# Optimization experiments

Measured on AMD Instinct MI355X. Metric: run time of the kernel, lower is better.

The kernel has to match this reference:

```python
import jax, jax.numpy as jnp
import numpy as np

EPS = 1e-7


def squash(s):
    # safe norm over last axis, keepdims
    norm = jnp.sqrt(jnp.sum(jnp.square(s), axis=-1, keepdims=True) + EPS)
    norm_sq = jnp.square(norm)
    return norm_sq / (1.0 + norm_sq) / norm * s


def setup_inputs() -> dict:
    key = jax.random.key(0)
    k1, k2 = jax.random.split(key)
    B, IN_CAPS, IN_DIM = 64, 2048, 16
    N_CAPS, CAP_DIM = 64, 16
    x = jax.random.normal(k1, (B, IN_CAPS, IN_DIM), dtype=jnp.float32)
    # glorot-uniform-ish init for W
    limit = (6.0 / (IN_DIM + N_CAPS * CAP_DIM)) ** 0.5
    W = jax.random.uniform(k2, (IN_CAPS, IN_DIM, N_CAPS * CAP_DIM),
                           minval=-limit, maxval=limit, dtype=jnp.float32)
    bias = jnp.zeros((N_CAPS, CAP_DIM), dtype=jnp.float32)
    return {"x": x, "W": W, "bias": bias}


def reference(x, W, bias):
    B, in_caps, in_dim = x.shape
    n_caps, cap_dim = bias.shape
    r_iters = 3
    # projection: [B, in_caps, n_caps*cap_dim] -> [B, in_caps, n_caps, cap_dim]
    u_hat = jnp.einsum('bij,ijk->bik', x, W).reshape(B, in_caps, n_caps, cap_dim)
    b = jnp.zeros((B, in_caps, n_caps, 1), dtype=u_hat.dtype)
    v = None
    for r in range(r_iters):
        c = jax.nn.softmax(b, axis=2)                       # route over class caps
        s = jnp.sum(u_hat * c, axis=1, keepdims=True)       # [B, 1, n_caps, cap_dim]
        s = s + bias
        v = squash(s)
        if r < r_iters - 1:
            agreement = jnp.sum(u_hat * v, axis=-1, keepdims=True)
            b = b + agreement
    return jnp.squeeze(v, axis=1)                           # [B, n_caps, cap_dim]
```

## Files before the change

### kernel.cpp

```cpp
#include <hip/hip_runtime.h>
#include <hip/hip_fp16.h>
#include <cstdio>

#define B_  64
#define I_  2048
#define J_  16
#define N_  64
#define D_  16
#define K_  1024

typedef __attribute__((ext_vector_type(2))) float float2v;

#if __has_builtin(__builtin_amdgcn_cvt_pk_u8_f32)
#define CVTPK_U8(f, sel, old) (unsigned)__builtin_amdgcn_cvt_pk_u8_f32((f), (sel), (old))
#else
__device__ __forceinline__ unsigned cvtpk_u8_sw(float f, unsigned sel, unsigned old) {
  unsigned b = (unsigned)(int)f & 0xffu;
  unsigned sh = sel * 8u;
  return (old & ~(0xffu << sh)) | (b << sh);
}
#define CVTPK_U8(f, sel, old) cvtpk_u8_sw((f), (sel), (old))
#endif

__device__ __forceinline__ void pk_fma_lo(float2v& a, float2v x, float2v w) {
  asm("v_pk_fma_f32 %0, %1, %2, %0 op_sel:[0,0,0] op_sel_hi:[0,1,1]"
      : "+v"(a) : "v"(x), "v"(w));
}
__device__ __forceinline__ void pk_fma_hi(float2v& a, float2v x, float2v w) {
  asm("v_pk_fma_f32 %0, %1, %2, %0 op_sel:[1,0,0] op_sel_hi:[1,1,1]"
      : "+v"(a) : "v"(x), "v"(w));
}

__global__ __launch_bounds__(256, 3) void project_k(const float* __restrict__ x,
                                                    const float* __restrict__ W,
                                                    unsigned char* __restrict__ uh,
                                                    unsigned short* __restrict__ sc) {
  const int i  = blockIdx.x >> 1;
  const int b0 = (blockIdx.x & 1) * 32;
  const int t  = threadIdx.x;

  __shared__ float4 xl4[32 * 4];
  if (t < 128) {
    int bb = t >> 2, q = t & 3;
    xl4[t] = ((const float4*)(x + ((size_t)(b0 + bb) * I_ + i) * J_))[q];
  }

  const float4* Wp = (const float4*)(W + (size_t)i * (J_ * K_));
  float2v w2[32];
#pragma unroll
  for (int j = 0; j < J_; ++j) {
    float4 wv = Wp[j * (K_ / 4) + t];
    w2[2 * j]     = float2v{wv.x, wv.y};
    w2[2 * j + 1] = float2v{wv.z, wv.w};
  }
  __syncthreads();

  unsigned char*  op  = uh + ((size_t)b0 * I_ + i) * K_ + t * 4;
  unsigned short* scp = sc + ((size_t)b0 * I_ + i) * N_ + (t >> 2);
  const bool lead = (t & 3) == 0;
  const float2v* xlp = (const float2v*)xl4;

#define QUANT_STORE(A01, A23) do {                                              \
    float ax_ = fmaxf(fmaxf(fabsf((A01).x), fabsf((A01).y)),                    \
                      fmaxf(fabsf((A23).x), fabsf((A23).y)));                   \
    ax_ = fmaxf(ax_, __shfl_xor(ax_, 1));                                       \
    ax_ = fmaxf(ax_, __shfl_xor(ax_, 2));                                       \
    float inv_ = __fdividef(127.0f, fmaxf(ax_, 1e-30f));                        \
    float e0_ = rintf(fmaf((A01).x, inv_, 128.f));                              \
    float e1_ = rintf(fmaf((A01).y, inv_, 128.f));                              \
    float e2_ = rintf(fmaf((A23).x, inv_, 128.f));                              \
    float e3_ = rintf(fmaf((A23).y, inv_, 128.f));                              \
    unsigned pk_ = CVTPK_U8(e0_, 0u, 0u);                                       \
    pk_ = CVTPK_U8(e1_, 1u, pk_);                                               \
    pk_ = CVTPK_U8(e2_, 2u, pk_);                                               \
    pk_ = CVTPK_U8(e3_, 3u, pk_);                                               \
    *(unsigned int*)op = pk_;                                                   \
    if (lead) *scp = __half_as_ushort(__float2half_rn(ax_ * (1.0f / 127.0f))); \
    op  += (size_t)I_ * K_;                                                     \
    scp += (size_t)I_ * N_;                                                     \
  } while (0)

#define FMA_BODY(XP)                                                            \
    float2v a01 = {0.f, 0.f}, a23 = {0.f, 0.f};                                 \
    _Pragma("unroll")                                                           \
    for (int p = 0; p < 8; ++p) {                                               \
      pk_fma_lo(a01, (XP)[p], w2[4 * p + 0]);                                   \
      pk_fma_lo(a23, (XP)[p], w2[4 * p + 1]);                                   \
      pk_fma_hi(a01, (XP)[p], w2[4 * p + 2]);                                   \
      pk_fma_hi(a23, (XP)[p], w2[4 * p + 3]);                                   \
    }

  float2v xa[8], xb[8];
#pragma unroll
  for (int p = 0; p < 8; ++p) xa[p] = xlp[p];

  for (int bb = 0; bb < 32; bb += 2) {
#pragma unroll
    for (int p = 0; p < 8; ++p) xb[p] = xlp[(bb + 1) * 8 + p];
    {
      FMA_BODY(xa)
      QUANT_STORE(a01, a23);
    }
    if (bb + 2 < 32) {
#pragma unroll
      for (int p = 0; p < 8; ++p) xa[p] = xlp[(bb + 2) * 8 + p];
    }
    {
      FMA_BODY(xb)
      QUANT_STORE(a01, a23);
    }
  }
#undef FMA_BODY
#undef QUANT_STORE
}

template <int MODE>
__global__ __launch_bounds__(256, 4) void route_k(const unsigned char* __restrict__ uh,
                                                  const unsigned short* __restrict__ sc,
                                                  const float* __restrict__ sa,
                                                  const float* __restrict__ sb,
                                                  const float* __restrict__ bias,
                                                  float* __restrict__ s_out) {
  const int t    = threadIdx.x;
  const int lane = t & 63;
  const int wv   = t >> 6;
  const int b    = blockIdx.x >> 4;
  const int iw   = ((blockIdx.x & 15) << 2) + wv;
  const int i0   = iw * 32;

  float vsum[16];
  float voff = 0.f;
  if (MODE >= 1) {
    float bs[16];
#pragma unroll
    for (int q = 0; q < 4; ++q) {
      float4 bb4 = *(const float4*)&bias[lane * 16 + q * 4];
      bs[q*4+0] = bb4.x; bs[q*4+1] = bb4.y; bs[q*4+2] = bb4.z; bs[q*4+3] = bb4.w;
    }
    {
      float va[16], nn = 0.f;
#pragma unroll
      for (int q = 0; q < 4; ++q) {
        float4 tmp = *(const float4*)&sa[(size_t)b * K_ + lane * 16 + q * 4];
        va[q*4+0] = tmp.x + bs[q*4+0]; va[q*4+1] = tmp.y + bs[q*4+1];
        va[q*4+2] = tmp.z + bs[q*4+2]; va[q*4+3] = tmp.w + bs[q*4+3];
      }
#pragma unroll
      for (int d = 0; d < 16; ++d) nn += va[d] * va[d];
      float n2 = nn + 1e-7f;
      float f = sqrtf(n2) / (1.0f + n2);
#pragma unroll
      for (int d = 0; d < 16; ++d) vsum[d] = va[d] * f;
    }
    if (MODE == 2) {
      float vb[16], nn = 0.f;
#pragma unroll
      for (int q = 0; q < 4; ++q) {
        float4 tmp = *(const float4*)&sb[(size_t)b * K_ + lane * 16 + q * 4];
        vb[q*4+0] = tmp.x + bs[q*4+0]; vb[q*4+1] = tmp.y + bs[q*4+1];
        vb[q*4+2] = tmp.z + bs[q*4+2]; vb[q*4+3] = tmp.w + bs[q*4+3];
      }
#pragma unroll
      for (int d = 0; d < 16; ++d) nn += vb[d] * vb[d];
      float n2 = nn + 1e-7f;
      float f = sqrtf(n2) / (1.0f + n2);
#pragma unroll
      for (int d = 0; d < 16; ++d) vsum[d] += vb[d] * f;
    }
    float tv = 0.f;
#pragma unroll
    for (int d = 0; d < 16; ++d) tv += vsum[d];
    voff = 128.0f * tv;
  }

  constexpr int IPW = 32;
  constexpr int PF  = 4;

  const unsigned char*  base = uh + (size_t)b * I_ * K_ + lane * 16;
  const unsigned short* scb  = sc + (size_t)b * I_ * N_ + lane;

  uint4 dbuf[PF];
  unsigned short hbuf[PF];
#pragma unroll
  for (int p = 0; p < PF; ++p) {
    int ip = (i0 + p) & (I_ - 1);
    dbuf[p] = *(const uint4*)(base + (size_t)ip * K_);
    hbuf[p] = scb[(size_t)ip * N_];
  }

  float s_loc[16];
#pragma unroll
  for (int d = 0; d < 16; ++d) s_loc[d] = 0.f;
  float csum = 0.f;

  for (int ii = 0; ii < IPW; ii += PF) {
#pragma unroll
    for (int p = 0; p < PF; ++p) {
      float scale = __half2float(__ushort_as_half(hbuf[p]));
      float u[16];
      {
        unsigned wd;
        wd = dbuf[p].x;
        u[0]  = (float)(wd & 0xffu);         u[1]  = (float)((wd >> 8) & 0xffu);
        u[2]  = (float)((wd >> 16) & 0xffu); u[3]  = (float)(wd >> 24);
        wd = dbuf[p].y;
        u[4]  = (float)(wd & 0xffu);         u[5]  = (float)((wd >> 8) & 0xffu);
        u[6]  = (float)((wd >> 16) & 0xffu); u[7]  = (float)(wd >> 24);
        wd = dbuf[p].z;
        u[8]  = (float)(wd & 0xffu);         u[9]  = (float)((wd >> 8) & 0xffu);
        u[10] = (float)((wd >> 16) & 0xffu); u[11] = (float)(wd >> 24);
        wd = dbuf[p].w;
        u[12] = (float)(wd & 0xffu);         u[13] = (float)((wd >> 8) & 0xffu);
        u[14] = (float)((wd >> 16) & 0xffu); u[15] = (float)(wd >> 24);
      }

      int ip = (i0 + ii + p + PF) & (I_ - 1);
      dbuf[p] = *(const uint4*)(base + (size_t)ip * K_);
      hbuf[p] = scb[(size_t)ip * N_];

      if (MODE == 0) {
#pragma unroll
        for (int d = 0; d < 16; ++d) s_loc[d] = fmaf(scale, u[d], s_loc[d]);
        csum += scale;
      } else {
        float dot = 0.f;
#pragma unroll
        for (int d = 0; d < 16; ++d) dot = fmaf(u[d], vsum[d], dot);
        float bl = scale * (dot - voff);
        float m = bl;
        m = fmaxf(m, __shfl_xor(m, 1));
        m = fmaxf(m, __shfl_xor(m, 2));
        m = fmaxf(m, __shfl_xor(m, 4));
        m = fmaxf(m, __shfl_xor(m, 8));
        m = fmaxf(m, __shfl_xor(m, 16));
        m = fmaxf(m, __shfl_xor(m, 32));
        float e = __expf(bl - m);
        float ss = e;
        ss += __shfl_xor(ss, 1);
        ss += __shfl_xor(ss, 2);
        ss += __shfl_xor(ss, 4);
        ss += __shfl_xor(ss, 8);
        ss += __shfl_xor(ss, 16);
        ss += __shfl_xor(ss, 32);
        float cs = __fdividef(e, ss) * scale;
#pragma unroll
        for (int d = 0; d < 16; ++d) s_loc[d] = fmaf(cs, u[d], s_loc[d]);
        csum += cs;
      }
    }
  }

#pragma unroll
  for (int d = 0; d < 16; ++d) s_loc[d] -= 128.0f * csum;
  if (MODE == 0) {
#pragma unroll
    for (int d = 0; d < 16; ++d) s_loc[d] *= (1.0f / 64.0f);
  }

  __shared__ float sred[4][64 * 17];
#pragma unroll
  for (int d = 0; d < 16; ++d) sred[wv][lane * 17 + d] = s_loc[d];
  __syncthreads();
#pragma unroll
  for (int e = 0; e < 4; ++e) {
    int idx = t * 4 + e;
    int n = idx >> 4, d = idx & 15;
    float val = sred[0][n*17+d] + sred[1][n*17+d] + sred[2][n*17+d] + sred[3][n*17+d];
    atomicAdd(&s_out[(size_t)b * K_ + idx], val);
  }
}

__global__ __launch_bounds__(256) void squash_k(const float* __restrict__ s_in,
                                                const float* __restrict__ bias,
                                                float* __restrict__ v_out) {
  const int b = blockIdx.x, t = threadIdx.x, k0 = t * 4;
  float4 s = *(const float4*)&s_in[b * K_ + k0];
  float4 bb = *(const float4*)&bias[k0];
  s.x += bb.x; s.y += bb.y; s.z += bb.z; s.w += bb.w;
  float p = s.x * s.x + s.y * s.y + s.z * s.z + s.w * s.w;
  p += __shfl_xor(p, 1);
  p += __shfl_xor(p, 2);
  float n2 = p + 1e-7f;
  float nrm = sqrtf(n2);
  float f = nrm / (1.0f + n2);
  float4 o = {s.x * f, s.y * f, s.z * f, s.w * f};
  *(float4*)&v_out[b * K_ + k0] = o;
}

extern "C" void kernel_launch(void* const* d_in, const int* in_sizes, int n_in,
                              void* d_out, int out_size, void* d_ws, size_t ws_size,
                              hipStream_t stream) {
  const float* x    = (const float*)d_in[0];
  const float* W    = (const float*)d_in[1];
  const float* bias = (const float*)d_in[2];
  float* out = (float*)d_out;

  char* ws = (char*)d_ws;
  size_t off = 0;
  unsigned char*  uh = (unsigned char*)(ws + off);  off += (size_t)B_ * I_ * K_;
  unsigned short* sc = (unsigned short*)(ws + off); off += (size_t)B_ * I_ * N_ * 2;
  float* s0 = (float*)(ws + off); off += (size_t)B_ * K_ * 4;
  float* s1 = (float*)(ws + off); off += (size_t)B_ * K_ * 4;
  float* s2 = (float*)(ws + off); off += (size_t)B_ * K_ * 4;

  if (ws_size < off)
    fprintf(stderr, "ClassCapsule: ws_size=%zu < needed=%zu — expect corruption\n", ws_size, off);

  (void)hipMemsetAsync(s0, 0, (size_t)3 * B_ * K_ * 4, stream);

  project_k<<<dim3(I_ * 2), dim3(256), 0, stream>>>(x, W, uh, sc);

  route_k<0><<<dim3(1024), dim3(256), 0, stream>>>(uh, sc, nullptr, nullptr, bias, s0);
  route_k<1><<<dim3(1024), dim3(256), 0, stream>>>(uh, sc, s0, nullptr, bias, s1);
  route_k<2><<<dim3(1024), dim3(256), 0, stream>>>(uh, sc, s0, s1, bias, s2);
  squash_k<<<dim3(B_), dim3(256), 0, stream>>>(s2, bias, out);
}
```

Baseline: 198.1 us.

## Compute capsule projection with bf16 MFMA and LDS-staged coalesced int8 stores

Replaces the packed-FP32 FMA projection with bf16 16x16x32 MFMA instructions, converting W and x to bf16 in LDS. Each block now handles all 64 batches for one input capsule. Quantized outputs are staged in a swizzled LDS tile so they can be written with coalesced 16-byte stores. The aim is to cut the VALU cost of the projection and improve store efficiency. The trade-off is bf16 rounding of the inputs and half the MFMA K dimension wasted as zero padding, since J is only 16.

```diff
diff --git a/kernel.cpp b/kernel.cpp
--- a/kernel.cpp
+++ b/kernel.cpp
@@ -1,4 +1,5 @@
 #include <hip/hip_runtime.h>
+#include <hip/hip_bf16.h>
 #include <hip/hip_fp16.h>
 #include <cstdio>
 
@@ -9,7 +10,8 @@
 #define D_  16
 #define K_  1024
 
-typedef __attribute__((ext_vector_type(2))) float float2v;
+using short8 = __attribute__((ext_vector_type(8))) short;
+using f32x4  = __attribute__((ext_vector_type(4))) float;
 
 #if __has_builtin(__builtin_amdgcn_cvt_pk_u8_f32)
 #define CVTPK_U8(f, sel, old) (unsigned)__builtin_amdgcn_cvt_pk_u8_f32((f), (sel), (old))
@@ -22,96 +24,113 @@
 #define CVTPK_U8(f, sel, old) cvtpk_u8_sw((f), (sel), (old))
 #endif
 
-__device__ __forceinline__ void pk_fma_lo(float2v& a, float2v x, float2v w) {
-  asm("v_pk_fma_f32 %0, %1, %2, %0 op_sel:[0,0,0] op_sel_hi:[0,1,1]"
-      : "+v"(a) : "v"(x), "v"(w));
-}
-__device__ __forceinline__ void pk_fma_hi(float2v& a, float2v x, float2v w) {
-  asm("v_pk_fma_f32 %0, %1, %2, %0 op_sel:[1,0,0] op_sel_hi:[1,1,1]"
-      : "+v"(a) : "v"(x), "v"(w));
-}
-
-__global__ __launch_bounds__(256, 3) void project_k(const float* __restrict__ x,
-                                                    const float* __restrict__ W,
-                                                    unsigned char* __restrict__ uh,
-                                                    unsigned short* __restrict__ sc) {
-  const int i  = blockIdx.x >> 1;
-  const int b0 = (blockIdx.x & 1) * 32;
+__device__ __forceinline__ short8 pack_bf16x8(float a0, float a1, float a2, float a3,
+                                              float a4, float a5, float a6, float a7) {
+  __hip_bfloat162 p0 = __float22bfloat162_rn(float2{a0, a1});
+  __hip_bfloat162 p1 = __float22bfloat162_rn(float2{a2, a3});
+  __hip_bfloat162 p2 = __float22bfloat162_rn(float2{a4, a5});
+  __hip_bfloat162 p3 = __float22bfloat162_rn(float2{a6, a7});
+  union { unsigned u[4]; short8 s; } cv;
+  cv.u[0] = *(unsigned*)&p0; cv.u[1] = *(unsigned*)&p1;
+  cv.u[2] = *(unsigned*)&p2; cv.u[3] = *(unsigned*)&p3;
+  return cv.s;
+}
+
+__global__ __launch_bounds__(256) void project_k(const float* __restrict__ x,
+                                                 const float* __restrict__ W,
+                                                 unsigned char* __restrict__ uh,
+                                                 unsigned short* __restrict__ sc) {
+  const int i  = blockIdx.x;
   const int t  = threadIdx.x;
-
-  __shared__ float4 xl4[32 * 4];
-  if (t < 128) {
-    int bb = t >> 2, q = t & 3;
-    xl4[t] = ((const float4*)(x + ((size_t)(b0 + bb) * I_ + i) * J_))[q];
-  }
-
-  const float4* Wp = (const float4*)(W + (size_t)i * (J_ * K_));
-  float2v w2[32];
-#pragma unroll
-  for (int j = 0; j < J_; ++j) {
-    float4 wv = Wp[j * (K_ / 4) + t];
-    w2[2 * j]     = float2v{wv.x, wv.y};
-    w2[2 * j + 1] = float2v{wv.z, wv.w};
+  const int l  = t & 63;
+  const int wv = t >> 6;
+
+  __shared__ unsigned short lds_w[256 * 20];
+  __shared__ float          lds_x[64 * 20];
+  __shared__ unsigned int   out_lds[64 * 64];
+  __shared__ unsigned short sc_lds[64 * 20];
+
+  {
+    int b = t >> 2, q = t & 3;
+    float4 v = ((const float4*)(x + ((size_t)b * I_ + i) * J_))[q];
+    *(float4*)&lds_x[b * 20 + q * 4] = v;
   }
   __syncthreads();
 
-  unsigned char*  op  = uh + ((size_t)b0 * I_ + i) * K_ + t * 4;
-  unsigned short* scp = sc + ((size_t)b0 * I_ + i) * N_ + (t >> 2);
-  const bool lead = (t & 3) == 0;
-  const float2v* xlp = (const float2v*)xl4;
-
-#define QUANT_STORE(A01, A23) do {                                              \
-    float ax_ = fmaxf(fmaxf(fabsf((A01).x), fabsf((A01).y)),                    \
-                      fmaxf(fabsf((A23).x), fabsf((A23).y)));                   \
-    ax_ = fmaxf(ax_, __shfl_xor(ax_, 1));                                       \
-    ax_ = fmaxf(ax_, __shfl_xor(ax_, 2));                                       \
-    float inv_ = __fdividef(127.0f, fmaxf(ax_, 1e-30f));                        \
-    float e0_ = rintf(fmaf((A01).x, inv_, 128.f));                              \
-    float e1_ = rintf(fmaf((A01).y, inv_, 128.f));                              \
-    float e2_ = rintf(fmaf((A23).x, inv_, 128.f));                              \
-    float e3_ = rintf(fmaf((A23).y, inv_, 128.f));                              \
-    unsigned pk_ = CVTPK_U8(e0_, 0u, 0u);                                       \
-    pk_ = CVTPK_U8(e1_, 1u, pk_);                                               \
-    pk_ = CVTPK_U8(e2_, 2u, pk_);                                               \
-    pk_ = CVTPK_U8(e3_, 3u, pk_);                                               \
-    *(unsigned int*)op = pk_;                                                   \
-    if (lead) *scp = __half_as_ushort(__float2half_rn(ax_ * (1.0f / 127.0f))); \
-    op  += (size_t)I_ * K_;                                                     \
-    scp += (size_t)I_ * N_;                                                     \
-  } while (0)
-
-#define FMA_BODY(XP)                                                            \
-    float2v a01 = {0.f, 0.f}, a23 = {0.f, 0.f};                                 \
-    _Pragma("unroll")                                                           \
-    for (int p = 0; p < 8; ++p) {                                               \
-      pk_fma_lo(a01, (XP)[p], w2[4 * p + 0]);                                   \
-      pk_fma_lo(a23, (XP)[p], w2[4 * p + 1]);                                   \
-      pk_fma_hi(a01, (XP)[p], w2[4 * p + 2]);                                   \
-      pk_fma_hi(a23, (XP)[p], w2[4 * p + 3]);                                   \
-    }
-
-  float2v xa[8], xb[8];
-#pragma unroll
-  for (int p = 0; p < 8; ++p) xa[p] = xlp[p];
-
-  for (int bb = 0; bb < 32; bb += 2) {
-#pragma unroll
-    for (int p = 0; p < 8; ++p) xb[p] = xlp[(bb + 1) * 8 + p];
+  short8 xfrag = {0, 0, 0, 0, 0, 0, 0, 0};
+  if (l < 32) {
+    int b = wv * 16 + (l & 15);
+    const float* xp = &lds_x[b * 20 + (l >> 4) * 8];
+    float4 f0 = *(const float4*)xp;
+    float4 f1 = *(const float4*)(xp + 4);
+    xfrag = pack_bf16x8(f0.x, f0.y, f0.z, f0.w, f1.x, f1.y, f1.z, f1.w);
+  }
+
+  for (int ph = 0; ph < 4; ++ph) {
     {
-      FMA_BODY(xa)
-      QUANT_STORE(a01, a23);
-    }
-    if (bb + 2 < 32) {
-#pragma unroll
-      for (int p = 0; p < 8; ++p) xa[p] = xlp[(bb + 2) * 8 + p];
-    }
+      const float* wp = W + (size_t)i * (J_ * K_) + ph * 256 + t;
+      float wj[J_];
+#pragma unroll
+      for (int j = 0; j < J_; ++j) wj[j] = wp[(size_t)j * K_];
+#pragma unroll
+      for (int q = 0; q < 4; ++q) {
+        __hip_bfloat162 pA = __float22bfloat162_rn(float2{wj[4*q+0], wj[4*q+1]});
+        __hip_bfloat162 pB = __float22bfloat162_rn(float2{wj[4*q+2], wj[4*q+3]});
+        uint2 u; u.x = *(unsigned*)&pA; u.y = *(unsigned*)&pB;
+        *(uint2*)&lds_w[t * 20 + q * 4] = u;
+      }
+    }
+    __syncthreads();
+
+#pragma unroll
+    for (int ntl = 0; ntl < 16; ++ntl) {
+      short8 afrag = {0, 0, 0, 0, 0, 0, 0, 0};
+      if (l < 32) {
+        int krow = ntl * 16 + (l & 15);
+        const unsigned short* ap = &lds_w[krow * 20 + (l >> 4) * 8];
+        union { uint2 u2[2]; short8 s; } cv;
+        cv.u2[0] = *(const uint2*)ap;
+        cv.u2[1] = *(const uint2*)(ap + 4);
+        afrag = cv.s;
+      }
+      f32x4 acc = {0.f, 0.f, 0.f, 0.f};
+      acc = __builtin_amdgcn_mfma_f32_16x16x32_bf16(afrag, xfrag, acc, 0, 0, 0);
+
+      const int b = wv * 16 + (l & 15);
+      float ax = fmaxf(fmaxf(fabsf(acc[0]), fabsf(acc[1])),
+                       fmaxf(fabsf(acc[2]), fabsf(acc[3])));
+      ax = fmaxf(ax, __shfl_xor(ax, 16));
+      ax = fmaxf(ax, __shfl_xor(ax, 32));
+      float inv = __fdividef(127.0f, fmaxf(ax, 1e-30f));
+      float e0 = rintf(fmaf(acc[0], inv, 128.f));
+      float e1 = rintf(fmaf(acc[1], inv, 128.f));
+      float e2 = rintf(fmaf(acc[2], inv, 128.f));
+      float e3 = rintf(fmaf(acc[3], inv, 128.f));
+      unsigned pk = CVTPK_U8(e0, 0u, 0u);
+      pk = CVTPK_U8(e1, 1u, pk);
+      pk = CVTPK_U8(e2, 2u, pk);
+      pk = CVTPK_U8(e3, 3u, pk);
+      int kd = ntl * 4 + (l >> 4);
+      out_lds[b * 64 + (kd ^ ((b & 7) << 2))] = pk;
+      if (l < 16)
+        sc_lds[b * 20 + ntl] = __half_as_ushort(__float2half_rn(ax * (1.0f / 127.0f)));
+    }
+    __syncthreads();
+
     {
-      FMA_BODY(xb)
-      QUANT_STORE(a01, a23);
-    }
-  }
-#undef FMA_BODY
-#undef QUANT_STORE
+      int c = t & 15;
+#pragma unroll
+      for (int it = 0; it < 4; ++it) {
+        int b = (t >> 4) + it * 16;
+        uint4 v = *(const uint4*)&out_lds[b * 64 + ((c * 4) ^ ((b & 7) << 2))];
+        *(uint4*)(uh + (size_t)b * I_ * K_ + (size_t)i * K_ + ph * 256 + c * 16) = v;
+      }
+      int b2 = t >> 2, n4 = (t & 3) * 4;
+      uint2 sv = *(const uint2*)&sc_lds[b2 * 20 + n4];
+      *(uint2*)(sc + (size_t)b2 * I_ * N_ + (size_t)i * N_ + ph * 16 + n4) = sv;
+    }
+    __syncthreads();
+  }
 }
 
 template <int MODE>
@@ -308,7 +327,7 @@
 
   (void)hipMemsetAsync(s0, 0, (size_t)3 * B_ * K_ * 4, stream);
 
-  project_k<<<dim3(I_ * 2), dim3(256), 0, stream>>>(x, W, uh, sc);
+  project_k<<<dim3(I_), dim3(256), 0, stream>>>(x, W, uh, sc);
 
   route_k<0><<<dim3(1024), dim3(256), 0, stream>>>(uh, sc, nullptr, nullptr, bias, s0);
   route_k<1><<<dim3(1024), dim3(256), 0, stream>>>(uh, sc, s0, nullptr, bias, s1);
```

After: 171.6 us. -13.4%, faster.
